# Kernel optimization log

Measured on AMD Instinct MI355X. Metric: run time of the kernel, lower is better.

The kernel has to match this reference:

```python
import jax, jax.numpy as jnp
import numpy as np

V = 100          # atoms per molecule (reactant and every candidate product)
C = 1000         # number of candidate products (B - 1)
E_R = 250        # directed edges in reactant graph
E_P = C * E_R    # total edges over all candidate product graphs
NODE_IN = 82     # WLN atom feature size
EDGE_IN = 6      # WLN bond feature size
H = 128          # node_hidden_feats
N_LAYERS = 3     # num_encode_gnn_layers


def setup_inputs() -> dict:
    key = jax.random.key(0)
    ks = jax.random.split(key, 20)
    # reactant graph edges
    r_src = jax.random.randint(ks[0], (E_R,), 0, V)
    r_dst = jax.random.randint(ks[1], (E_R,), 0, V)
    # candidate product graphs: random edges within each graph, offset per graph
    p_src_local = jax.random.randint(ks[2], (C, E_R), 0, V)
    p_dst_local = jax.random.randint(ks[3], (C, E_R), 0, V)
    offsets = (jnp.arange(C) * V)[:, None]
    p_src = (p_src_local + offsets).reshape(-1)
    p_dst = (p_dst_local + offsets).reshape(-1)

    def rn(k, shape, scale=0.1):
        return jax.random.normal(k, shape, dtype=jnp.float32) * scale

    return dict(
        reactant_node_feats=rn(ks[4], (V, NODE_IN), 1.0),
        reactant_edge_feats=rn(ks[5], (E_R, EDGE_IN), 1.0),
        product_node_feats=rn(ks[6], (C * V, NODE_IN), 1.0),
        product_edge_feats=rn(ks[7], (E_P, EDGE_IN), 1.0),
        candidate_scores=rn(ks[8], (C, 1), 1.0),
        # shared-weight WLN encoder (used for both reactant and products)
        W_proj=rn(ks[9], (NODE_IN, H)), b_proj=jnp.zeros((H,), jnp.float32),
        W_msg=rn(ks[10], (H + EDGE_IN, H)), b_msg=jnp.zeros((H,), jnp.float32),
        W_new=rn(ks[11], (2 * H, H)), b_new=jnp.zeros((H,), jnp.float32),
        # diff WLN (1 layer, no input projection)
        W_msg_d=rn(ks[12], (H + EDGE_IN, H)), b_msg_d=jnp.zeros((H,), jnp.float32),
        W_new_d=rn(ks[13], (2 * H, H)), b_new_d=jnp.zeros((H,), jnp.float32),
        # prediction head
        W_pred1=rn(ks[14], (H, H)), b_pred1=jnp.zeros((H,), jnp.float32),
        W_pred2=rn(ks[15], (H, 1)), b_pred2=jnp.zeros((1,), jnp.float32),
        reactant_src=r_src, reactant_dst=r_dst,
        product_src=p_src, product_dst=p_dst,
    )


def _wln_layers(h, e, src, dst, n_nodes, W_msg, b_msg, W_new, b_new, n_layers):
    # dgllife WLN: message/update MLP weights are SHARED across the n_layers iterations.
    for _ in range(n_layers):
        # per-edge message: ReLU(Linear([h_src ; e]))  -- [E, H]
        m = jax.nn.relu(jnp.concatenate([h[src], e], axis=1) @ W_msg + b_msg)
        # scatter-sum messages to destination nodes -- [N, H]
        agg = jax.ops.segment_sum(m, dst, num_segments=n_nodes)
        # node update: ReLU(Linear([h ; agg]))
        h = jax.nn.relu(jnp.concatenate([h, agg], axis=1) @ W_new + b_new)
    return h


def reference(reactant_node_feats, reactant_edge_feats, product_node_feats,
              product_edge_feats, candidate_scores,
              W_proj, b_proj, W_msg, b_msg, W_new, b_new,
              W_msg_d, b_msg_d, W_new_d, b_new_d,
              W_pred1, b_pred1, W_pred2, b_pred2,
              reactant_src, reactant_dst, product_src, product_dst):
    # encoder WLN (project_in_feats=True, 3 shared-weight layers)
    r = jax.nn.relu(reactant_node_feats @ W_proj + b_proj)
    r = _wln_layers(r, reactant_edge_feats, reactant_src, reactant_dst, V,
                    W_msg, b_msg, W_new, b_new, N_LAYERS)            # [V, H]
    p = jax.nn.relu(product_node_feats @ W_proj + b_proj)
    p = _wln_layers(p, product_edge_feats, product_src, product_dst, C * V,
                    W_msg, b_msg, W_new, b_new, N_LAYERS)            # [C*V, H]
    # node-wise difference against broadcast reactant features
    diff = (p.reshape(C, V, H) - r[None, :, :]).reshape(-1, H)       # [C*V, H]
    # diff WLN (project_in_feats=False, 1 layer)
    d = _wln_layers(diff, product_edge_feats, product_src, product_dst, C * V,
                    W_msg_d, b_msg_d, W_new_d, b_new_d, 1)           # [C*V, H]
    # sum pooling per candidate graph (each graph has exactly V nodes)
    g = d.reshape(C, V, H).sum(axis=1)                               # [C, H]
    # MLP scorer + candidate scores
    return jax.nn.relu(g @ W_pred1 + b_pred1) @ W_pred2 + b_pred2 + candidate_scores
```

## Files before the change

### kernel.cpp

```cpp
#include <hip/hip_runtime.h>
#include <hip/hip_bf16.h>
#include <cstdint>

#define H 128
#define VV 100
#define CC 1000
#define ER_N 250
#define NODE_IN_N 82
#define EDGE_IN_N 6
#define LDA 136
#define NT 512
#define NP_TOT 100000

typedef short short8 __attribute__((ext_vector_type(8)));
typedef float floatx4 __attribute__((ext_vector_type(4)));
typedef __hip_bfloat16 bf16;

#define OFF_B0 0
#define OFF_B1 27200
#define OFF_EF 54400
#define OFF_RP 62400
#define OFF_CNT 62816
#define OFF_SD 63232
#define OFF_EIDX 64240
#define OFF_RED 65248
#define OFF_G 67296
#define SMEM_TOTAL 67808

#define PREP_W (27 * 4096)
#define PREP_X (NP_TOT * 48)
__global__ __launch_bounds__(256) void prep_all(
    const float* __restrict__ Wp, const float* __restrict__ Wm,
    const float* __restrict__ Wn, const float* __restrict__ Wmd,
    const float* __restrict__ Wnd, const float* __restrict__ Xp,
    const float* __restrict__ Epe,
    bf16* __restrict__ wfrag, bf16* __restrict__ Xbf, float* __restrict__ Epad,
    int* __restrict__ flag) {
  long idx = (long)blockIdx.x * 256 + threadIdx.x;
  if (idx == 0) *flag = 0;
  if (idx < PREP_W) {
    const float* W;
    int Ksrc;
    long local = idx;
    if (idx < 3 * 4096)       { W = Wp;  Ksrc = NODE_IN_N; }
    else if (idx < 7 * 4096)  { W = Wm;  Ksrc = H;     local -= 3 * 4096; }
    else if (idx < 15 * 4096) { W = Wn;  Ksrc = 2 * H; local -= 7 * 4096; }
    else if (idx < 19 * 4096) { W = Wmd; Ksrc = H;     local -= 15 * 4096; }
    else                      { W = Wnd; Ksrc = 2 * H; local -= 19 * 4096; }
    int j = local & 7, lane = (local >> 3) & 63, nt = (local >> 9) & 7, kc = local >> 12;
    int k = kc * 32 + ((lane >> 4) & 3) * 8 + j;
    int n = nt * 16 + (lane & 15);
    float v = (k < Ksrc) ? W[(size_t)k * H + n] : 0.f;
    wfrag[idx] = __float2bfloat16(v);
    return;
  }
  idx -= PREP_W;
  if (idx < (long)PREP_X) {
    long r = idx / 48;
    int p = (int)(idx - r * 48);
    int c0 = 2 * p;
    float v0 = (c0 < NODE_IN_N) ? Xp[r * NODE_IN_N + c0] : 0.f;
    float v1 = (c0 + 1 < NODE_IN_N) ? Xp[r * NODE_IN_N + c0 + 1] : 0.f;
    __hip_bfloat162 pk;
    pk.x = __float2bfloat16(v0);
    pk.y = __float2bfloat16(v1);
    *(__hip_bfloat162*)&Xbf[r * 96 + c0] = pk;
    return;
  }
  idx -= (long)PREP_X;
  if (idx < (long)NP_TOT * 20) {
    long e = idx >> 3;
    int k = (int)(idx & 7);
    Epad[idx] = (k < EDGE_IN_N) ? Epe[e * EDGE_IN_N + k] : 0.f;
  }
}

template<int CHUNKS>
__device__ __forceinline__ void load_bfrag(short8 b[CHUNKS], const bf16* __restrict__ Wf,
                                           int nt8, int lane) {
#pragma unroll
  for (int kc = 0; kc < CHUNKS; ++kc)
    b[kc] = *(const short8*)(Wf + ((size_t)((kc * 8 + nt8) * 64 + lane)) * 8);
}

template<int CHUNKS>
__device__ __forceinline__ void mfma_m7(floatx4 acc[7], const short8 b[CHUNKS],
                                        const bf16* A, int l16, int quad) {
#pragma unroll
  for (int kc = 0; kc < CHUNKS; ++kc)
#pragma unroll
    for (int mi = 0; mi < 7; ++mi) {
      short8 a = *(const short8*)(A + (mi * 16 + l16) * LDA + kc * 32 + quad * 8);
      acc[mi] = __builtin_amdgcn_mfma_f32_16x16x32_bf16(a, b[kc], acc[mi], 0, 0, 0);
    }
}

__device__ __forceinline__ void epi(floatx4 acc[7], const float* __restrict__ bias,
                                    bool relu, bf16* Out, int nt8, int quad, int l16) {
  int col = nt8 * 16 + l16;
  float bb = bias[col];
#pragma unroll
  for (int mi = 0; mi < 7; ++mi)
#pragma unroll
    for (int r = 0; r < 4; ++r) {
      int row = mi * 16 + quad * 4 + r;
      if (row < VV) {
        float v = acc[mi][r] + bb;
        if (relu) v = fmaxf(v, 0.f);
        Out[row * LDA + col] = __float2bfloat16(v);
      }
    }
}

__device__ __forceinline__ void zero7(floatx4 acc[7]) {
#pragma unroll
  for (int mi = 0; mi < 7; ++mi) acc[mi] = (floatx4){0.f, 0.f, 0.f, 0.f};
}

__device__ __forceinline__ void gather(const bf16* Y, bf16* X, const float* sEf,
                                       const int* sRowPtr, const int* sEidx,
                                       const float* __restrict__ WmBot,
                                       int q8, int c2) {
  float wb[EDGE_IN_N][2];
#pragma unroll
  for (int k = 0; k < EDGE_IN_N; ++k) {
    float2 w2 = *(const float2*)&WmBot[k * H + 2 * c2];
    wb[k][0] = w2.x;
    wb[k][1] = w2.y;
  }
#pragma unroll
  for (int i = 0; i < 13; ++i) {
    int n = q8 + 8 * i;
    if (n < VV) {
      int p0 = sRowPtr[n], p1 = sRowPtr[n + 1];
      float a0 = 0.f, a1 = 0.f;
      for (int p = p0; p < p1; ++p) {
        int v = sEidx[p];
        int s = v & 127, e = v >> 7;
        uint32_t tt = *(const uint32_t*)&Y[s * LDA + 2 * c2];
        float u0 = __uint_as_float((tt & 0xffffu) << 16);
        float u1 = __uint_as_float((tt >> 16) << 16);
        float4 ea = *(const float4*)&sEf[e * 8];
        float2 eb = *(const float2*)&sEf[e * 8 + 4];
        u0 = fmaf(ea.x, wb[0][0], u0); u1 = fmaf(ea.x, wb[0][1], u1);
        u0 = fmaf(ea.y, wb[1][0], u0); u1 = fmaf(ea.y, wb[1][1], u1);
        u0 = fmaf(ea.z, wb[2][0], u0); u1 = fmaf(ea.z, wb[2][1], u1);
        u0 = fmaf(ea.w, wb[3][0], u0); u1 = fmaf(ea.w, wb[3][1], u1);
        u0 = fmaf(eb.x, wb[4][0], u0); u1 = fmaf(eb.x, wb[4][1], u1);
        u0 = fmaf(eb.y, wb[5][0], u0); u1 = fmaf(eb.y, wb[5][1], u1);
        a0 += fmaxf(u0, 0.f);
        a1 += fmaxf(u1, 0.f);
      }
      __hip_bfloat162 pk;
      pk.x = __float2bfloat16(a0);
      pk.y = __float2bfloat16(a1);
      *(__hip_bfloat162*)&X[n * LDA + 2 * c2] = pk;
    }
  }
}

__device__ __forceinline__ void wln_layer(
    bf16* X, bf16* Y, const float* sEf, const int* sRowPtr, const int* sEidx,
    const bf16* __restrict__ wf_msg, const float* __restrict__ bmsg,
    const float* __restrict__ WmBot,
    const bf16* __restrict__ wf_new, const float* __restrict__ bnew,
    int lane, int nt8, int quad, int l16, int q8, int c2) {
  short8 bm_[4], bu1[4], bu2[4];
  floatx4 accM[7], accU[7];
  load_bfrag<4>(bm_, wf_msg, nt8, lane);
  zero7(accM);
  mfma_m7<4>(accM, bm_, X, l16, quad);
  load_bfrag<4>(bu1, wf_new, nt8, lane);
  epi(accM, bmsg, false, Y, nt8, quad, l16);
  __syncthreads();
  zero7(accU);
  mfma_m7<4>(accU, bu1, X, l16, quad);
  load_bfrag<4>(bu2, wf_new + 4 * 4096, nt8, lane);
  __syncthreads();
  gather(Y, X, sEf, sRowPtr, sEidx, WmBot, q8, c2);
  __syncthreads();
  mfma_m7<4>(accU, bu2, X, l16, quad);
  epi(accU, bnew, true, Y, nt8, quad, l16);
  __syncthreads();
}

__global__ __launch_bounds__(NT, 4) void wln_fused(
    const float* __restrict__ Xr, const float* __restrict__ Ere,
    const int* __restrict__ rsrc, const int* __restrict__ rdst,
    const bf16* __restrict__ Xbf, const float* __restrict__ Epad,
    const int* __restrict__ psrc, const int* __restrict__ pdst,
    const bf16* __restrict__ wf_proj, const float* __restrict__ bproj,
    const bf16* __restrict__ wf_msg, const float* __restrict__ bmsg,
    const float* __restrict__ WmBot,
    const bf16* __restrict__ wf_new, const float* __restrict__ bnew,
    const bf16* __restrict__ wf_msgd, const float* __restrict__ bmsgd,
    const float* __restrict__ WmdBot,
    const bf16* __restrict__ wf_newd, const float* __restrict__ bnewd,
    bf16* __restrict__ hr_global, int* __restrict__ flag,
    const float* __restrict__ W1, const float* __restrict__ b1,
    const float* __restrict__ W2, const float* __restrict__ b2,
    const float* __restrict__ scores, float* __restrict__ out) {
  __shared__ __align__(16) char smem[SMEM_TOTAL];
  bf16* sB0 = (bf16*)(smem + OFF_B0);
  bf16* sB1 = (bf16*)(smem + OFF_B1);
  float* sEf = (float*)(smem + OFF_EF);
  int* sRowPtr = (int*)(smem + OFF_RP);
  int* sCnt = (int*)(smem + OFF_CNT);
  int* sSD = (int*)(smem + OFF_SD);
  int* sEidx = (int*)(smem + OFF_EIDX);
  float* sRed = (float*)(smem + OFF_RED);
  float* sG = (float*)(smem + OFF_G);

  const int tid = threadIdx.x;
  const int lane = tid & 63;
  const int wave = tid >> 6;
  const int quad = (lane >> 4) & 3, l16 = lane & 15;
  const int nt8 = wave;
  const int q8 = tid >> 6, c2 = tid & 63;
  const bool REAC = (blockIdx.x == 0);
  const int c = REAC ? 0 : (blockIdx.x - 1);
  const int no = c * VV;
  const long eo = (long)c * ER_N;

  if (tid < VV) sCnt[tid] = 0;
  __syncthreads();
  if (tid < ER_N) {
    int s, d;
    if (REAC) { s = rsrc[tid]; d = rdst[tid]; }
    else      { s = psrc[eo + tid] - no; d = pdst[eo + tid] - no; }
    sSD[tid] = (d << 16) | s;
    atomicAdd(&sCnt[d], 1);
  }
  if (!REAC) {
    const float4* Ep = (const float4*)(Epad + eo * 8);
    for (int f = tid; f < 500; f += NT) ((float4*)sEf)[f] = Ep[f];
    const bf16* Xb = Xbf + (size_t)no * 96;
    for (int f = tid; f < 1200; f += NT) {
      int r = f / 12, g = f - r * 12;
      *(float4*)&sB0[r * LDA + g * 8] = *(const float4*)(Xb + r * 96 + g * 8);
    }
  } else {
    for (int f = tid; f < ER_N * EDGE_IN_N; f += NT) {
      int e = f / EDGE_IN_N, k = f - e * EDGE_IN_N;
      sEf[e * 8 + k] = Ere[f];
    }
    for (int f = tid; f < VV * 96; f += NT) {
      int r = f / 96, cc = f - r * 96;
      float v = (cc < NODE_IN_N) ? Xr[r * NODE_IN_N + cc] : 0.f;
      sB0[r * LDA + cc] = __float2bfloat16(v);
    }
  }
  __syncthreads();

  if (wave == 0) {
    int c0 = sCnt[lane];
    int c1 = (lane + 64 < VV) ? sCnt[lane + 64] : 0;
    int v = c0;
#pragma unroll
    for (int d = 1; d < 64; d <<= 1) {
      int t = __shfl_up(v, d, 64);
      if (lane >= d) v += t;
    }
    int total0 = __shfl(v, 63, 64);
    int w = c1;
#pragma unroll
    for (int d = 1; d < 64; d <<= 1) {
      int t = __shfl_up(w, d, 64);
      if (lane >= d) w += t;
    }
    int ex0 = v - c0;
    int ex1 = total0 + w - c1;
    sRowPtr[lane] = ex0;
    sCnt[lane] = ex0;
    if (lane + 64 < VV) {
      sRowPtr[lane + 64] = ex1;
      sCnt[lane + 64] = ex1;
    }
    if (lane == 0) sRowPtr[VV] = ER_N;
  }
  __syncthreads();
  if (tid < ER_N) {
    int sd = sSD[tid];
    int p = atomicAdd(&sCnt[sd >> 16], 1);
    sEidx[p] = (sd & 0xffff) | (tid << 7);
  }
  __syncthreads();

  {
    short8 bp_[3];
    floatx4 acc[7];
    load_bfrag<3>(bp_, wf_proj, nt8, lane);
    zero7(acc);
    mfma_m7<3>(acc, bp_, sB0, l16, quad);
    epi(acc, bproj, true, sB1, nt8, quad, l16);
  }
  __syncthreads();

  bf16* Hb = sB1;
  bf16* Tb = sB0;

  for (int l = 0; l < 3; ++l) {
    wln_layer(Hb, Tb, sEf, sRowPtr, sEidx, wf_msg, bmsg, WmBot, wf_new, bnew,
              lane, nt8, quad, l16, q8, c2);
    bf16* tmp = Hb; Hb = Tb; Tb = tmp;
  }

  if (REAC) {
    for (int f = tid; f < VV * H / 2; f += NT) {
      int r = f >> 6, j = (f & 63) * 2;
      uint32_t pk = *(const uint32_t*)&Hb[r * LDA + j];
      __hip_atomic_store((uint32_t*)hr_global + f, pk,
                         __ATOMIC_RELAXED, __HIP_MEMORY_SCOPE_AGENT);
    }
    __syncthreads();
    if (tid == 0)
      __hip_atomic_store(flag, 1, __ATOMIC_RELEASE, __HIP_MEMORY_SCOPE_AGENT);
    return;
  }

  if (tid == 0) {
    while (__hip_atomic_load(flag, __ATOMIC_ACQUIRE, __HIP_MEMORY_SCOPE_AGENT) == 0)
      __builtin_amdgcn_s_sleep(16);
  }
  __syncthreads();
  for (int f = tid; f < VV * H / 2; f += NT) {
    int r = f >> 6, j = (f & 63) * 2;
    uint32_t rk = __hip_atomic_load((const uint32_t*)hr_global + f,
                                    __ATOMIC_RELAXED, __HIP_MEMORY_SCOPE_AGENT);
    uint32_t hk = *(const uint32_t*)&Hb[r * LDA + j];
    float h0 = __uint_as_float((hk & 0xffffu) << 16) -
               __uint_as_float((rk & 0xffffu) << 16);
    float h1 = __uint_as_float((hk >> 16) << 16) -
               __uint_as_float((rk >> 16) << 16);
    __hip_bfloat162 o;
    o.x = __float2bfloat16(h0);
    o.y = __float2bfloat16(h1);
    *(__hip_bfloat162*)&Hb[r * LDA + j] = o;
  }
  __syncthreads();

  wln_layer(Hb, Tb, sEf, sRowPtr, sEidx, wf_msgd, bmsgd, WmdBot, wf_newd, bnewd,
            lane, nt8, quad, l16, q8, c2);
  { bf16* tmp = Hb; Hb = Tb; Tb = tmp; }

  {
    int j = tid & 127, qq = tid >> 7;
    float p = 0.f;
    for (int v = qq * 25; v < qq * 25 + 25; ++v)
      p += __bfloat162float(Hb[v * LDA + j]);
    sRed[tid] = p;
  }
  __syncthreads();
  if (tid < H) {
    float s = 0.f;
#pragma unroll
    for (int q = 0; q < 4; ++q) s += sRed[q * 128 + tid];
    sG[tid] = s;
  }
  __syncthreads();
  {
    int j = tid & 127, qq = tid >> 7;
    float a = 0.f;
    for (int k = qq * 32; k < qq * 32 + 32; ++k)
      a = fmaf(sG[k], W1[(size_t)k * H + j], a);
    sRed[tid] = a;
  }
  __syncthreads();
  if (tid < H) {
    float m = b1[tid];
#pragma unroll
    for (int q = 0; q < 4; ++q) m += sRed[q * 128 + tid];
    sG[tid] = fmaxf(m, 0.f) * W2[tid];
  }
  __syncthreads();
  if (wave == 0) {
    float v = sG[lane] + sG[lane + 64];
#pragma unroll
    for (int d = 32; d > 0; d >>= 1) v += __shfl_down(v, d, 64);
    if (lane == 0) out[c] = v + b2[0] + scores[c];
  }
}

extern "C" void kernel_launch(void* const* d_in, const int* in_sizes, int n_in,
                              void* d_out, int out_size, void* d_ws, size_t ws_size,
                              hipStream_t stream) {
  const float* Xr  = (const float*)d_in[0];
  const float* Ere = (const float*)d_in[1];
  const float* Xp  = (const float*)d_in[2];
  const float* Epe = (const float*)d_in[3];
  const float* sc  = (const float*)d_in[4];
  const float* Wp  = (const float*)d_in[5];
  const float* bp  = (const float*)d_in[6];
  const float* Wm  = (const float*)d_in[7];
  const float* bm  = (const float*)d_in[8];
  const float* Wn  = (const float*)d_in[9];
  const float* bn  = (const float*)d_in[10];
  const float* Wmd = (const float*)d_in[11];
  const float* bmd = (const float*)d_in[12];
  const float* Wnd = (const float*)d_in[13];
  const float* bnd = (const float*)d_in[14];
  const float* W1  = (const float*)d_in[15];
  const float* b1  = (const float*)d_in[16];
  const float* W2  = (const float*)d_in[17];
  const float* b2  = (const float*)d_in[18];
  const int* rsrc  = (const int*)d_in[19];
  const int* rdst  = (const int*)d_in[20];
  const int* psrc  = (const int*)d_in[21];
  const int* pdst  = (const int*)d_in[22];

  bf16* wf_proj = (bf16*)d_ws;
  bf16* wf_msg  = wf_proj + 3 * 4096;
  bf16* wf_new  = wf_msg + 4 * 4096;
  bf16* wf_msgd = wf_new + 8 * 4096;
  bf16* wf_newd = wf_msgd + 4 * 4096;
  bf16* hr      = wf_newd + 8 * 4096;
  bf16* Xbf     = hr + VV * H;
  float* Epad   = (float*)(Xbf + (size_t)NP_TOT * 96);
  int* flag     = (int*)(Epad + (size_t)250000 * 8);

  float* out = (float*)d_out;

  {
    long total = (long)PREP_W + (long)PREP_X + (long)NP_TOT * 20;
    int blocks = (int)((total + 255) / 256);
    prep_all<<<blocks, 256, 0, stream>>>(Wp, Wm, Wn, Wmd, Wnd, Xp, Epe,
                                         wf_proj, Xbf, Epad, flag);
  }

  wln_fused<<<CC + 1, NT, 0, stream>>>(
      Xr, Ere, rsrc, rdst, Xbf, Epad, psrc, pdst,
      wf_proj, bp, wf_msg, bm, Wm + H * H, wf_new, bn,
      wf_msgd, bmd, Wmd + H * H, wf_newd, bnd, hr, flag,
      W1, b1, W2, b2, sc, out);
}
```

Before: 280.7 us.

## Drop bf16/edge prepack pass and retile MFMA work as 4x2 wave grid

Removes the prep pass that converted all product node features to padded bf16 and padded edge features in global memory. The fused kernel now reads the fp32 inputs directly, converting and padding them in shared memory. This avoids a full extra write-plus-read of the large product feature arrays. Separately, the MFMA work is redistributed so each wave computes 4 (or 3) row tiles times 2 column tiles instead of 7 row tiles times 1 column tile, which changes register use and how A-fragments are reused across waves. The risk is that the in-kernel loads are uncoalesced (scalar fp32 rather than float4), and the new partition gives unequal work to the two wave halves.

```diff
diff --git a/kernel.cpp b/kernel.cpp
--- a/kernel.cpp
+++ b/kernel.cpp
@@ -10,7 +10,6 @@
 #define EDGE_IN_N 6
 #define LDA 136
 #define NT 512
-#define NP_TOT 100000
 
 typedef short short8 __attribute__((ext_vector_type(8)));
 typedef float floatx4 __attribute__((ext_vector_type(4)));
@@ -28,93 +27,81 @@
 #define SMEM_TOTAL 67808
 
 #define PREP_W (27 * 4096)
-#define PREP_X (NP_TOT * 48)
-__global__ __launch_bounds__(256) void prep_all(
+__global__ __launch_bounds__(256) void prep_w(
     const float* __restrict__ Wp, const float* __restrict__ Wm,
     const float* __restrict__ Wn, const float* __restrict__ Wmd,
-    const float* __restrict__ Wnd, const float* __restrict__ Xp,
-    const float* __restrict__ Epe,
-    bf16* __restrict__ wfrag, bf16* __restrict__ Xbf, float* __restrict__ Epad,
+    const float* __restrict__ Wnd, bf16* __restrict__ wfrag,
     int* __restrict__ flag) {
-  long idx = (long)blockIdx.x * 256 + threadIdx.x;
+  int idx = blockIdx.x * 256 + threadIdx.x;
   if (idx == 0) *flag = 0;
-  if (idx < PREP_W) {
-    const float* W;
-    int Ksrc;
-    long local = idx;
-    if (idx < 3 * 4096)       { W = Wp;  Ksrc = NODE_IN_N; }
-    else if (idx < 7 * 4096)  { W = Wm;  Ksrc = H;     local -= 3 * 4096; }
-    else if (idx < 15 * 4096) { W = Wn;  Ksrc = 2 * H; local -= 7 * 4096; }
-    else if (idx < 19 * 4096) { W = Wmd; Ksrc = H;     local -= 15 * 4096; }
-    else                      { W = Wnd; Ksrc = 2 * H; local -= 19 * 4096; }
-    int j = local & 7, lane = (local >> 3) & 63, nt = (local >> 9) & 7, kc = local >> 12;
-    int k = kc * 32 + ((lane >> 4) & 3) * 8 + j;
-    int n = nt * 16 + (lane & 15);
-    float v = (k < Ksrc) ? W[(size_t)k * H + n] : 0.f;
-    wfrag[idx] = __float2bfloat16(v);
-    return;
-  }
-  idx -= PREP_W;
-  if (idx < (long)PREP_X) {
-    long r = idx / 48;
-    int p = (int)(idx - r * 48);
-    int c0 = 2 * p;
-    float v0 = (c0 < NODE_IN_N) ? Xp[r * NODE_IN_N + c0] : 0.f;
-    float v1 = (c0 + 1 < NODE_IN_N) ? Xp[r * NODE_IN_N + c0 + 1] : 0.f;
-    __hip_bfloat162 pk;
-    pk.x = __float2bfloat16(v0);
-    pk.y = __float2bfloat16(v1);
-    *(__hip_bfloat162*)&Xbf[r * 96 + c0] = pk;
-    return;
-  }
-  idx -= (long)PREP_X;
-  if (idx < (long)NP_TOT * 20) {
-    long e = idx >> 3;
-    int k = (int)(idx & 7);
-    Epad[idx] = (k < EDGE_IN_N) ? Epe[e * EDGE_IN_N + k] : 0.f;
-  }
+  if (idx >= PREP_W) return;
+  const float* W;
+  int Ksrc, local = idx;
+  if (idx < 3 * 4096)       { W = Wp;  Ksrc = NODE_IN_N; }
+  else if (idx < 7 * 4096)  { W = Wm;  Ksrc = H;     local -= 3 * 4096; }
+  else if (idx < 15 * 4096) { W = Wn;  Ksrc = 2 * H; local -= 7 * 4096; }
+  else if (idx < 19 * 4096) { W = Wmd; Ksrc = H;     local -= 15 * 4096; }
+  else                      { W = Wnd; Ksrc = 2 * H; local -= 19 * 4096; }
+  int j = local & 7, lane = (local >> 3) & 63, nt = (local >> 9) & 7, kc = local >> 12;
+  int k = kc * 32 + ((lane >> 4) & 3) * 8 + j;
+  int n = nt * 16 + (lane & 15);
+  float v = (k < Ksrc) ? W[(size_t)k * H + n] : 0.f;
+  wfrag[idx] = __float2bfloat16(v);
 }
 
 template<int CHUNKS>
-__device__ __forceinline__ void load_bfrag(short8 b[CHUNKS], const bf16* __restrict__ Wf,
-                                           int nt8, int lane) {
+__device__ __forceinline__ void load_b2(short8 b[2][CHUNKS], const bf16* __restrict__ Wf,
+                                        int gh, int lane) {
+#pragma unroll
+  for (int kc = 0; kc < CHUNKS; ++kc) {
+    b[0][kc] = *(const short8*)(Wf + ((size_t)((kc * 8 + 2 * gh + 0) * 64 + lane)) * 8);
+    b[1][kc] = *(const short8*)(Wf + ((size_t)((kc * 8 + 2 * gh + 1) * 64 + lane)) * 8);
+  }
+}
+
+template<int CHUNKS>
+__device__ __forceinline__ void mfma_g(floatx4 acc[4][2], const short8 b[2][CHUNKS],
+                                       const bf16* A, int m0, int mc,
+                                       int l16, int quad) {
 #pragma unroll
   for (int kc = 0; kc < CHUNKS; ++kc)
-    b[kc] = *(const short8*)(Wf + ((size_t)((kc * 8 + nt8) * 64 + lane)) * 8);
-}
-
-template<int CHUNKS>
-__device__ __forceinline__ void mfma_m7(floatx4 acc[7], const short8 b[CHUNKS],
-                                        const bf16* A, int l16, int quad) {
-#pragma unroll
-  for (int kc = 0; kc < CHUNKS; ++kc)
-#pragma unroll
-    for (int mi = 0; mi < 7; ++mi) {
-      short8 a = *(const short8*)(A + (mi * 16 + l16) * LDA + kc * 32 + quad * 8);
-      acc[mi] = __builtin_amdgcn_mfma_f32_16x16x32_bf16(a, b[kc], acc[mi], 0, 0, 0);
-    }
-}
-
-__device__ __forceinline__ void epi(floatx4 acc[7], const float* __restrict__ bias,
-                                    bool relu, bf16* Out, int nt8, int quad, int l16) {
-  int col = nt8 * 16 + l16;
-  float bb = bias[col];
-#pragma unroll
-  for (int mi = 0; mi < 7; ++mi)
-#pragma unroll
-    for (int r = 0; r < 4; ++r) {
-      int row = mi * 16 + quad * 4 + r;
-      if (row < VV) {
-        float v = acc[mi][r] + bb;
-        if (relu) v = fmaxf(v, 0.f);
-        Out[row * LDA + col] = __float2bfloat16(v);
+#pragma unroll
+    for (int mi = 0; mi < 4; ++mi)
+      if (mi < mc) {
+        short8 a = *(const short8*)(A + ((m0 + mi) * 16 + l16) * LDA + kc * 32 + quad * 8);
+        acc[mi][0] = __builtin_amdgcn_mfma_f32_16x16x32_bf16(a, b[0][kc], acc[mi][0], 0, 0, 0);
+        acc[mi][1] = __builtin_amdgcn_mfma_f32_16x16x32_bf16(a, b[1][kc], acc[mi][1], 0, 0, 0);
       }
-    }
-}
-
-__device__ __forceinline__ void zero7(floatx4 acc[7]) {
-#pragma unroll
-  for (int mi = 0; mi < 7; ++mi) acc[mi] = (floatx4){0.f, 0.f, 0.f, 0.f};
+}
+
+__device__ __forceinline__ void epi2(floatx4 acc[4][2], const float* __restrict__ bias,
+                                     bool relu, bf16* Out,
+                                     int gh, int m0, int mc, int quad, int l16) {
+#pragma unroll
+  for (int nn = 0; nn < 2; ++nn) {
+    int col = (2 * gh + nn) * 16 + l16;
+    float bb = bias[col];
+#pragma unroll
+    for (int mi = 0; mi < 4; ++mi)
+      if (mi < mc)
+#pragma unroll
+        for (int r = 0; r < 4; ++r) {
+          int row = (m0 + mi) * 16 + quad * 4 + r;
+          if (row < VV) {
+            float v = acc[mi][nn][r] + bb;
+            if (relu) v = fmaxf(v, 0.f);
+            Out[row * LDA + col] = __float2bfloat16(v);
+          }
+        }
+  }
+}
+
+__device__ __forceinline__ void zero42(floatx4 acc[4][2]) {
+#pragma unroll
+  for (int mi = 0; mi < 4; ++mi) {
+    acc[mi][0] = (floatx4){0.f, 0.f, 0.f, 0.f};
+    acc[mi][1] = (floatx4){0.f, 0.f, 0.f, 0.f};
+  }
 }
 
 __device__ __forceinline__ void gather(const bf16* Y, bf16* X, const float* sEf,
@@ -164,30 +151,30 @@
     const bf16* __restrict__ wf_msg, const float* __restrict__ bmsg,
     const float* __restrict__ WmBot,
     const bf16* __restrict__ wf_new, const float* __restrict__ bnew,
-    int lane, int nt8, int quad, int l16, int q8, int c2) {
-  short8 bm_[4], bu1[4], bu2[4];
-  floatx4 accM[7], accU[7];
-  load_bfrag<4>(bm_, wf_msg, nt8, lane);
-  zero7(accM);
-  mfma_m7<4>(accM, bm_, X, l16, quad);
-  load_bfrag<4>(bu1, wf_new, nt8, lane);
-  epi(accM, bmsg, false, Y, nt8, quad, l16);
-  __syncthreads();
-  zero7(accU);
-  mfma_m7<4>(accU, bu1, X, l16, quad);
-  load_bfrag<4>(bu2, wf_new + 4 * 4096, nt8, lane);
+    int lane, int gh, int m0, int mc, int quad, int l16, int q8, int c2) {
+  short8 bm_[2][4], bu1[2][4], bu2[2][4];
+  floatx4 accM[4][2], accU[4][2];
+  load_b2<4>(bm_, wf_msg, gh, lane);
+  zero42(accM);
+  mfma_g<4>(accM, bm_, X, m0, mc, l16, quad);
+  load_b2<4>(bu1, wf_new, gh, lane);
+  epi2(accM, bmsg, false, Y, gh, m0, mc, quad, l16);
+  __syncthreads();
+  zero42(accU);
+  mfma_g<4>(accU, bu1, X, m0, mc, l16, quad);
+  load_b2<4>(bu2, wf_new + 4 * 4096, gh, lane);
   __syncthreads();
   gather(Y, X, sEf, sRowPtr, sEidx, WmBot, q8, c2);
   __syncthreads();
-  mfma_m7<4>(accU, bu2, X, l16, quad);
-  epi(accU, bnew, true, Y, nt8, quad, l16);
+  mfma_g<4>(accU, bu2, X, m0, mc, l16, quad);
+  epi2(accU, bnew, true, Y, gh, m0, mc, quad, l16);
   __syncthreads();
 }
 
 __global__ __launch_bounds__(NT, 4) void wln_fused(
     const float* __restrict__ Xr, const float* __restrict__ Ere,
     const int* __restrict__ rsrc, const int* __restrict__ rdst,
-    const bf16* __restrict__ Xbf, const float* __restrict__ Epad,
+    const float* __restrict__ Xp, const float* __restrict__ Epe,
     const int* __restrict__ psrc, const int* __restrict__ pdst,
     const bf16* __restrict__ wf_proj, const float* __restrict__ bproj,
     const bf16* __restrict__ wf_msg, const float* __restrict__ bmsg,
@@ -215,7 +202,8 @@
   const int lane = tid & 63;
   const int wave = tid >> 6;
   const int quad = (lane >> 4) & 3, l16 = lane & 15;
-  const int nt8 = wave;
+  const int gh = wave & 3, mh = wave >> 2;
+  const int m0 = mh * 4, mc = mh ? 3 : 4;
   const int q8 = tid >> 6, c2 = tid & 63;
   const bool REAC = (blockIdx.x == 0);
   const int c = REAC ? 0 : (blockIdx.x - 1);
@@ -231,23 +219,20 @@
     sSD[tid] = (d << 16) | s;
     atomicAdd(&sCnt[d], 1);
   }
-  if (!REAC) {
-    const float4* Ep = (const float4*)(Epad + eo * 8);
-    for (int f = tid; f < 500; f += NT) ((float4*)sEf)[f] = Ep[f];
-    const bf16* Xb = Xbf + (size_t)no * 96;
-    for (int f = tid; f < 1200; f += NT) {
-      int r = f / 12, g = f - r * 12;
-      *(float4*)&sB0[r * LDA + g * 8] = *(const float4*)(Xb + r * 96 + g * 8);
-    }
-  } else {
+  {
+    const float* Xsrc = REAC ? Xr : (Xp + (size_t)no * NODE_IN_N);
+    const float* Esrc = REAC ? Ere : (Epe + (size_t)eo * EDGE_IN_N);
     for (int f = tid; f < ER_N * EDGE_IN_N; f += NT) {
       int e = f / EDGE_IN_N, k = f - e * EDGE_IN_N;
-      sEf[e * 8 + k] = Ere[f];
-    }
-    for (int f = tid; f < VV * 96; f += NT) {
-      int r = f / 96, cc = f - r * 96;
-      float v = (cc < NODE_IN_N) ? Xr[r * NODE_IN_N + cc] : 0.f;
-      sB0[r * LDA + cc] = __float2bfloat16(v);
+      sEf[e * 8 + k] = Esrc[f];
+    }
+    for (int f = tid; f < VV * NODE_IN_N; f += NT) {
+      int r = f / NODE_IN_N, cc = f - r * NODE_IN_N;
+      sB0[r * LDA + cc] = __float2bfloat16(Xsrc[f]);
+    }
+    for (int f = tid; f < VV * 14; f += NT) {
+      int r = f / 14, cc = NODE_IN_N + (f - r * 14);
+      sB0[r * LDA + cc] = __float2bfloat16(0.f);
     }
   }
   __syncthreads();
@@ -287,12 +272,12 @@
   __syncthreads();
 
   {
-    short8 bp_[3];
-    floatx4 acc[7];
-    load_bfrag<3>(bp_, wf_proj, nt8, lane);
-    zero7(acc);
-    mfma_m7<3>(acc, bp_, sB0, l16, quad);
-    epi(acc, bproj, true, sB1, nt8, quad, l16);
+    short8 bp_[2][3];
+    floatx4 acc[4][2];
+    load_b2<3>(bp_, wf_proj, gh, lane);
+    zero42(acc);
+    mfma_g<3>(acc, bp_, sB0, m0, mc, l16, quad);
+    epi2(acc, bproj, true, sB1, gh, m0, mc, quad, l16);
   }
   __syncthreads();
 
@@ -301,7 +286,7 @@
 
   for (int l = 0; l < 3; ++l) {
     wln_layer(Hb, Tb, sEf, sRowPtr, sEidx, wf_msg, bmsg, WmBot, wf_new, bnew,
-              lane, nt8, quad, l16, q8, c2);
+              lane, gh, m0, mc, quad, l16, q8, c2);
     bf16* tmp = Hb; Hb = Tb; Tb = tmp;
   }
 
@@ -340,7 +325,7 @@
   __syncthreads();
 
   wln_layer(Hb, Tb, sEf, sRowPtr, sEidx, wf_msgd, bmsgd, WmdBot, wf_newd, bnewd,
-            lane, nt8, quad, l16, q8, c2);
+            lane, gh, m0, mc, quad, l16, q8, c2);
   { bf16* tmp = Hb; Hb = Tb; Tb = tmp; }
 
   {
@@ -414,21 +399,15 @@
   bf16* wf_msgd = wf_new + 8 * 4096;
   bf16* wf_newd = wf_msgd + 4 * 4096;
   bf16* hr      = wf_newd + 8 * 4096;
-  bf16* Xbf     = hr + VV * H;
-  float* Epad   = (float*)(Xbf + (size_t)NP_TOT * 96);
-  int* flag     = (int*)(Epad + (size_t)250000 * 8);
+  int* flag     = (int*)(hr + VV * H);
 
   float* out = (float*)d_out;
 
-  {
-    long total = (long)PREP_W + (long)PREP_X + (long)NP_TOT * 20;
-    int blocks = (int)((total + 255) / 256);
-    prep_all<<<blocks, 256, 0, stream>>>(Wp, Wm, Wn, Wmd, Wnd, Xp, Epe,
-                                         wf_proj, Xbf, Epad, flag);
-  }
+  prep_w<<<(PREP_W + 255) / 256, 256, 0, stream>>>(Wp, Wm, Wn, Wmd, Wnd,
+                                                   wf_proj, flag);
 
   wln_fused<<<CC + 1, NT, 0, stream>>>(
-      Xr, Ere, rsrc, rdst, Xbf, Epad, psrc, pdst,
+      Xr, Ere, rsrc, rdst, Xp, Epe, psrc, pdst,
       wf_proj, bp, wf_msg, bm, Wm + H * H, wf_new, bn,
       wf_msgd, bmd, Wmd + H * H, wf_newd, bnd, hr, flag,
       W1, b1, W2, b2, sc, out);
```

Measured after the change: 348.5 us. 24.2% more time.
